# Performance work log

Measured on AMD Instinct MI355X. Metric: run time of the kernel, lower is better.

The kernel has to match this reference:

```python
import jax, jax.numpy as jnp
import numpy as np

B, N, F_IN, F_OUT = 8, 2048, 256, 256
NEG_SLOPE = 0.2
EPS = 1e-7


def setup_inputs() -> dict:
    key = jax.random.key(0)
    k1, k2, k3, k4, k5 = jax.random.split(key, 5)
    x = jax.random.normal(k1, (B, N, F_IN), dtype=jnp.float32)
    # A is a 0/1 adjacency mask used as float in the module
    A = jax.random.bernoulli(k2, 0.5, (B, N, N)).astype(jnp.float32)
    # W: xavier_normal_ init, shape [in_features, out_features]
    W = jax.random.normal(k3, (F_IN, F_OUT), dtype=jnp.float32) * np.sqrt(2.0 / (F_IN + F_OUT))
    # attention_mechanism: Linear(2*F_OUT, 1) -> weight vector [2*F_OUT], scalar bias
    bound = 1.0 / np.sqrt(2 * F_OUT)
    a_w = jax.random.uniform(k4, (2 * F_OUT,), dtype=jnp.float32, minval=-bound, maxval=bound)
    a_b = jax.random.uniform(k5, (), dtype=jnp.float32, minval=-bound, maxval=bound)
    return {"A": A, "x": x, "W": W, "a_w": a_w, "a_b": a_b}


def reference(A, x, W, a_w, a_b):
    # Wh = x @ W : [B, N, F_OUT]
    Wh = jnp.einsum('bnf,fo->bno', x, W)
    # Linear([Wh_i ; Wh_j]) == Wh_i @ a_w[:F] + Wh_j @ a_w[F:] + b  (no O(N^2 F) concat)
    s_src = Wh @ a_w[:F_OUT]   # [B, N] contribution of row index i
    s_dst = Wh @ a_w[F_OUT:]   # [B, N] contribution of col index j
    e = s_src[:, :, None] + s_dst[:, None, :] + a_b  # [B, N, N]
    e = jnp.where(e > 0, e, NEG_SLOPE * e)           # leaky_relu(0.2)
    # masked softmax over dim=1 (as in the original module)
    exps = jnp.exp(e) * A
    sums = jnp.sum(exps, axis=1, keepdims=True) + EPS
    attn = exps / sums                                # [B, N, N]
    return jnp.einsum('bij,bjo->bio', attn, Wh)       # [B, N, F_OUT]
```

## Files before the change

### kernel.cpp

```cpp
#include <hip/hip_runtime.h>
#include <hip/hip_bf16.h>

#define NN 2048
#define BB 8
#define FD 256
#define NEG_SLOPE 0.2f
#define EPSV 1e-7f
#define PSTR 36

typedef __bf16 bf16x8 __attribute__((ext_vector_type(8)));
typedef __bf16 bf16x4 __attribute__((ext_vector_type(4)));
typedef float f32x4 __attribute__((ext_vector_type(4)));

__device__ __forceinline__ void gload16(const __bf16* g, __bf16* l) {
    __builtin_amdgcn_global_load_lds((const __attribute__((address_space(1))) unsigned int*)g,
                                     (__attribute__((address_space(3))) unsigned int*)l,
                                     16, 0, 0);
}

__global__ __launch_bounds__(256) void k1_prep(const float* __restrict__ W,
                                               __bf16* __restrict__ WT) {
    int idx = blockIdx.x * 256 + threadIdx.x;
    int o = idx >> 8, f = idx & 255;
    WT[idx] = (__bf16)W[f * FD + o];
}

__global__ __launch_bounds__(256) void k2_whgemm(const float* __restrict__ x,
                                                 const __bf16* __restrict__ WT,
                                                 const float* __restrict__ a_w,
                                                 float* __restrict__ Wh,
                                                 float* __restrict__ s_src,
                                                 float* __restrict__ s_dst) {
    const int wave = threadIdx.x >> 6;
    const int lane = threadIdx.x & 63;
    const int row0 = blockIdx.x * 32 + (wave >> 1) * 16;
    const int ohalf = (wave & 1) * 128;
    const int m = lane & 15;
    const int quad = lane >> 4;
    const int row = row0 + m;
    const float* xrow = x + (size_t)row * FD + quad * 8;

    f32x4 acc[8];
#pragma unroll
    for (int n = 0; n < 8; ++n) acc[n] = (f32x4){0.f, 0.f, 0.f, 0.f};

    for (int k0 = 0; k0 < FD; k0 += 32) {
        float4 xa = *(const float4*)(xrow + k0);
        float4 xb = *(const float4*)(xrow + k0 + 4);
        bf16x8 af;
        af[0] = (__bf16)xa.x; af[1] = (__bf16)xa.y; af[2] = (__bf16)xa.z; af[3] = (__bf16)xa.w;
        af[4] = (__bf16)xb.x; af[5] = (__bf16)xb.y; af[6] = (__bf16)xb.z; af[7] = (__bf16)xb.w;
#pragma unroll
        for (int n = 0; n < 8; ++n) {
            int o = ohalf + n * 16 + m;
            bf16x8 bf = *(const bf16x8*)(WT + o * FD + k0 + quad * 8);
            acc[n] = __builtin_amdgcn_mfma_f32_16x16x32_bf16(af, bf, acc[n], 0, 0, 0);
        }
    }
#pragma unroll
    for (int n = 0; n < 8; ++n) {
        int o = ohalf + n * 16 + m;
#pragma unroll
        for (int r = 0; r < 4; ++r) {
            Wh[(size_t)(row0 + quad * 4 + r) * FD + o] = acc[n][r];
        }
    }

    float psrc[4] = {0.f, 0.f, 0.f, 0.f};
    float pdst[4] = {0.f, 0.f, 0.f, 0.f};
#pragma unroll
    for (int n = 0; n < 8; ++n) {
        int o = ohalf + n * 16 + m;
        float awS = a_w[o], awD = a_w[FD + o];
#pragma unroll
        for (int r = 0; r < 4; ++r) {
            psrc[r] += acc[n][r] * awS;
            pdst[r] += acc[n][r] * awD;
        }
    }
#pragma unroll
    for (int off = 1; off <= 8; off <<= 1) {
#pragma unroll
        for (int r = 0; r < 4; ++r) {
            psrc[r] += __shfl_xor(psrc[r], off, 64);
            pdst[r] += __shfl_xor(pdst[r], off, 64);
        }
    }
    __shared__ float sS[2][2][16], sD[2][2][16];
    if (m == 0) {
        int rp = wave >> 1, oh = wave & 1;
#pragma unroll
        for (int r = 0; r < 4; ++r) {
            sS[rp][oh][quad * 4 + r] = psrc[r];
            sD[rp][oh][quad * 4 + r] = pdst[r];
        }
    }
    __syncthreads();
    if (threadIdx.x < 32) {
        int rp = threadIdx.x >> 4, idx = threadIdx.x & 15;
        int orow = blockIdx.x * 32 + rp * 16 + idx;
        s_src[orow] = sS[rp][0][idx] + sS[rp][1][idx];
        s_dst[orow] = sD[rp][0][idx] + sD[rp][1][idx];
    }
}

__global__ __launch_bounds__(256) void k4_den(const float* __restrict__ A,
                                              const float* __restrict__ s_src,
                                              const float* __restrict__ s_dst,
                                              const float* __restrict__ a_bp,
                                              float* __restrict__ den_part) {
    const int blk = blockIdx.x;
    const int b = blk & 7;
    const int jhalf = (blk >> 3) & 1;
    const int isp = blk >> 4;
    const int i0 = isp * 32;
    const int j = jhalf * 1024 + threadIdx.x * 4;
    __shared__ float ss[32];
    if (threadIdx.x < 32) ss[threadIdx.x] = s_src[b * NN + i0 + threadIdx.x] + a_bp[0];
    __syncthreads();
    float4 sd = *(const float4*)(s_dst + b * NN + j);
    float ax = 0.f, ay = 0.f, az = 0.f, aw = 0.f;
    const float* Ap = A + ((size_t)b * NN + i0) * NN + j;
#pragma unroll 8
    for (int i = 0; i < 32; ++i) {
        float4 a = *(const float4*)(Ap + (size_t)i * NN);
        float si = ss[i];
        float e0 = si + sd.x; e0 = e0 > 0.f ? e0 : NEG_SLOPE * e0;
        float e1 = si + sd.y; e1 = e1 > 0.f ? e1 : NEG_SLOPE * e1;
        float e2 = si + sd.z; e2 = e2 > 0.f ? e2 : NEG_SLOPE * e2;
        float e3 = si + sd.w; e3 = e3 > 0.f ? e3 : NEG_SLOPE * e3;
        ax += a.x * __expf(e0);
        ay += a.y * __expf(e1);
        az += a.z * __expf(e2);
        aw += a.w * __expf(e3);
    }
    float4 r = (float4){ax, ay, az, aw};
    *(float4*)(den_part + (size_t)isp * (BB * NN) + b * NN + j) = r;
}

__global__ __launch_bounds__(256) void k5_wht(const float* __restrict__ Wh,
                                              const float* __restrict__ den_part,
                                              __bf16* __restrict__ WhT) {
    const int b = blockIdx.z;
    const int j0 = blockIdx.x * 64;
    const int o0 = blockIdx.y * 64;
    __shared__ float tile[64][65];
    __shared__ float invd[64];
    if (threadIdx.x < 64) {
        float s = 0.f;
        const float* dp = den_part + b * NN + j0 + threadIdx.x;
#pragma unroll 8
        for (int sI = 0; sI < 64; ++sI) s += dp[(size_t)sI * (BB * NN)];
        invd[threadIdx.x] = 1.f / (s + EPSV);
    }
    __syncthreads();
    int jr = threadIdx.x >> 4, oc = (threadIdx.x & 15) * 4;
#pragma unroll
    for (int p = 0; p < 4; ++p) {
        int jj = jr + p * 16;
        float4 v = *(const float4*)(Wh + (size_t)(b * NN + j0 + jj) * FD + o0 + oc);
        float s = invd[jj];
        tile[jj][oc + 0] = v.x * s;
        tile[jj][oc + 1] = v.y * s;
        tile[jj][oc + 2] = v.z * s;
        tile[jj][oc + 3] = v.w * s;
    }
    __syncthreads();
    int ow = threadIdx.x >> 4, jc = (threadIdx.x & 15) * 4;
#pragma unroll
    for (int p = 0; p < 4; ++p) {
        int o = ow + p * 16;
        bf16x4 wv;
        wv[0] = (__bf16)tile[jc + 0][o];
        wv[1] = (__bf16)tile[jc + 1][o];
        wv[2] = (__bf16)tile[jc + 2][o];
        wv[3] = (__bf16)tile[jc + 3][o];
        *(bf16x4*)(WhT + (size_t)(b * FD + o0 + o) * NN + j0 + jc) = wv;
    }
}

__global__ __launch_bounds__(256) void k6_out(const float* __restrict__ A,
                                              const __bf16* __restrict__ WhT,
                                              const float* __restrict__ s_src,
                                              const float* __restrict__ s_dst,
                                              const float* __restrict__ a_bp,
                                              float* __restrict__ out) {
    __shared__ __bf16 Pt[2][32 * PSTR];
    __shared__ __bf16 Bt[2][128 * 32];
    const int blk = blockIdx.x;
    const int b = blk & 7;
    const int r_ = blk >> 3;
    const int itile = r_ & 63;
    const int oh = r_ >> 6;
    const int i0 = itile * 32;
    const int o0 = oh * 128;
    const int t = threadIdx.x;
    const int w = t >> 6, lane = t & 63;
    const int m = lane & 15, quad = lane >> 4;
    const int wrow = w >> 1, wcol = w & 1;

    const int prow = t >> 3, pj = (t & 7) * 4;
    const float ssr = s_src[b * NN + i0 + prow] + a_bp[0];
    const float* Abase = A + ((size_t)(b * NN + i0 + prow)) * NN + pj;
    const float* sdbase = s_dst + b * NN + pj;
    __bf16* Pw = &Pt[0][0] + prow * PSTR + pj;
    const int pstep = 32 * PSTR;

    const __bf16* gB0 = WhT + ((size_t)(b * FD + o0 + w * 16 + (lane >> 2))) * NN + (lane & 3) * 8;
    const __bf16* gB1 = gB0 + (size_t)64 * NN;
    __bf16* lB0 = &Bt[0][0] + (w * 16) * 32;
    __bf16* lB1 = &Bt[0][0] + (w * 16 + 64) * 32;
    const int lstepB = 128 * 32;

    float4 a0 = *(const float4*)(Abase);
    float4 q0 = *(const float4*)(sdbase);
    gload16(gB0, lB0);
    gload16(gB1, lB1);

#define BUILD_P(dstbuf)                                                          \
    {                                                                            \
        bf16x4 pv; float e;                                                      \
        e = ssr + q0.x; e = e > 0.f ? e : NEG_SLOPE * e; pv[0] = (__bf16)(a0.x * __expf(e)); \
        e = ssr + q0.y; e = e > 0.f ? e : NEG_SLOPE * e; pv[1] = (__bf16)(a0.y * __expf(e)); \
        e = ssr + q0.z; e = e > 0.f ? e : NEG_SLOPE * e; pv[2] = (__bf16)(a0.z * __expf(e)); \
        e = ssr + q0.w; e = e > 0.f ? e : NEG_SLOPE * e; pv[3] = (__bf16)(a0.w * __expf(e)); \
        *(bf16x4*)(Pw + (dstbuf) * pstep) = pv;                                  \
    }

    BUILD_P(0)

    f32x4 acc[4];
#pragma unroll
    for (int n = 0; n < 4; ++n) acc[n] = (f32x4){0.f, 0.f, 0.f, 0.f};

    const __bf16* Pr = &Pt[0][0] + (wrow * 16 + m) * PSTR + quad * 8;
    const __bf16* Br = &Bt[0][0] + (wcol * 64 + m) * 32 + quad * 8;

    for (int kk = 0; kk < 64; ++kk) {
        __syncthreads();
        const int cur = kk & 1, nb = cur ^ 1;
        if (kk < 63) {
            gload16(gB0 + (kk + 1) * 32, lB0 + nb * lstepB);
            gload16(gB1 + (kk + 1) * 32, lB1 + nb * lstepB);
            a0 = *(const float4*)(Abase + (kk + 1) * 32);
            q0 = *(const float4*)(sdbase + (kk + 1) * 32);
        }
        const __bf16* Pk = Pr + cur * pstep;
        const __bf16* Bk = Br + cur * lstepB;
        bf16x8 af = *(const bf16x8*)(Pk);
#pragma unroll
        for (int n = 0; n < 4; ++n) {
            bf16x8 bfr = *(const bf16x8*)(Bk + n * 16 * 32);
            acc[n] = __builtin_amdgcn_mfma_f32_16x16x32_bf16(af, bfr, acc[n], 0, 0, 0);
        }
        if (kk < 63) BUILD_P(nb)
    }

#pragma unroll
    for (int n = 0; n < 4; ++n) {
        int o = o0 + wcol * 64 + n * 16 + m;
#pragma unroll
        for (int rr = 0; rr < 4; ++rr) {
            int orow = i0 + wrow * 16 + quad * 4 + rr;
            out[((size_t)b * NN + orow) * FD + o] = acc[n][rr];
        }
    }
#undef BUILD_P
}

extern "C" void kernel_launch(void* const* d_in, const int* in_sizes, int n_in,
                              void* d_out, int out_size, void* d_ws, size_t ws_size,
                              hipStream_t stream) {
    const float* A   = (const float*)d_in[0];
    const float* x   = (const float*)d_in[1];
    const float* W   = (const float*)d_in[2];
    const float* a_w = (const float*)d_in[3];
    const float* a_b = (const float*)d_in[4];
    float* out = (float*)d_out;

    char* ws = (char*)d_ws;
    __bf16* WT      = (__bf16*)ws;
    float*  Wh      = (float*)(ws + 131072);
    __bf16* WhT     = (__bf16*)(ws + 16908288);
    float*  s_src   = (float*)(ws + 25296896);
    float*  s_dst   = (float*)(ws + 25362432);
    float*  den_part= (float*)(ws + 25427968);

    k1_prep<<<256, 256, 0, stream>>>(W, WT);
    k2_whgemm<<<512, 256, 0, stream>>>(x, WT, a_w, Wh, s_src, s_dst);
    k4_den<<<1024, 256, 0, stream>>>(A, s_src, s_dst, a_b, den_part);
    k5_wht<<<dim3(32, 4, 8), 256, 0, stream>>>(Wh, den_part, WhT);
    k6_out<<<1024, 256, 0, stream>>>(A, WhT, s_src, s_dst, a_b, out);
}
```

Baseline: 297.8 us.

## Materialize bf16 attention matrix per batch pair and run separate tiled GEMM

```diff
diff --git a/kernel.cpp b/kernel.cpp
--- a/kernel.cpp
+++ b/kernel.cpp
@@ -6,7 +6,6 @@
 #define FD 256
 #define NEG_SLOPE 0.2f
 #define EPSV 1e-7f
-#define PSTR 36
 
 typedef __bf16 bf16x8 __attribute__((ext_vector_type(8)));
 typedef __bf16 bf16x4 __attribute__((ext_vector_type(4)));
@@ -104,15 +103,18 @@
     }
 }
 
-__global__ __launch_bounds__(256) void k4_den(const float* __restrict__ A,
-                                              const float* __restrict__ s_src,
-                                              const float* __restrict__ s_dst,
-                                              const float* __restrict__ a_bp,
-                                              float* __restrict__ den_part) {
+template <bool WD, bool WP>
+__global__ __launch_bounds__(256) void k4_t(const float* __restrict__ A,
+                                            const float* __restrict__ s_src,
+                                            const float* __restrict__ s_dst,
+                                            const float* __restrict__ a_bp,
+                                            float* __restrict__ den_part,
+                                            __bf16* __restrict__ P,
+                                            int bmask, int sh) {
     const int blk = blockIdx.x;
-    const int b = blk & 7;
-    const int jhalf = (blk >> 3) & 1;
-    const int isp = blk >> 4;
+    const int b = blk & bmask;
+    const int jhalf = (blk >> sh) & 1;
+    const int isp = blk >> (sh + 1);
     const int i0 = isp * 32;
     const int j = jhalf * 1024 + threadIdx.x * 4;
     __shared__ float ss[32];
@@ -121,7 +123,8 @@
     float4 sd = *(const float4*)(s_dst + b * NN + j);
     float ax = 0.f, ay = 0.f, az = 0.f, aw = 0.f;
     const float* Ap = A + ((size_t)b * NN + i0) * NN + j;
-#pragma unroll 8
+    __bf16* Pp = WP ? (P + ((size_t)b * NN + i0) * NN + j) : (__bf16*)0;
+#pragma unroll 4
     for (int i = 0; i < 32; ++i) {
         float4 a = *(const float4*)(Ap + (size_t)i * NN);
         float si = ss[i];
@@ -129,13 +132,22 @@
         float e1 = si + sd.y; e1 = e1 > 0.f ? e1 : NEG_SLOPE * e1;
         float e2 = si + sd.z; e2 = e2 > 0.f ? e2 : NEG_SLOPE * e2;
         float e3 = si + sd.w; e3 = e3 > 0.f ? e3 : NEG_SLOPE * e3;
-        ax += a.x * __expf(e0);
-        ay += a.y * __expf(e1);
-        az += a.z * __expf(e2);
-        aw += a.w * __expf(e3);
-    }
-    float4 r = (float4){ax, ay, az, aw};
-    *(float4*)(den_part + (size_t)isp * (BB * NN) + b * NN + j) = r;
+        float p0 = a.x * __expf(e0);
+        float p1 = a.y * __expf(e1);
+        float p2 = a.z * __expf(e2);
+        float p3 = a.w * __expf(e3);
+        if (WD) { ax += p0; ay += p1; az += p2; aw += p3; }
+        if (WP) {
+            bf16x4 pv;
+            pv[0] = (__bf16)p0; pv[1] = (__bf16)p1;
+            pv[2] = (__bf16)p2; pv[3] = (__bf16)p3;
+            *(bf16x4*)(Pp + (size_t)i * NN) = pv;
+        }
+    }
+    if (WD) {
+        float4 r = (float4){ax, ay, az, aw};
+        *(float4*)(den_part + (size_t)isp * (BB * NN) + b * NN + j) = r;
+    }
 }
 
 __global__ __launch_bounds__(256) void k5_wht(const float* __restrict__ Wh,
@@ -179,93 +191,81 @@
     }
 }
 
-__global__ __launch_bounds__(256) void k6_out(const float* __restrict__ A,
-                                              const __bf16* __restrict__ WhT,
-                                              const float* __restrict__ s_src,
-                                              const float* __restrict__ s_dst,
-                                              const float* __restrict__ a_bp,
-                                              float* __restrict__ out) {
-    __shared__ __bf16 Pt[2][32 * PSTR];
-    __shared__ __bf16 Bt[2][128 * 32];
+__global__ __launch_bounds__(256) void k6_gemm(const __bf16* __restrict__ P,
+                                               const __bf16* __restrict__ WhT,
+                                               float* __restrict__ out,
+                                               int bmask, int bsh) {
+    __shared__ __bf16 lA[2][64 * 64];
+    __shared__ __bf16 lB[2][128 * 64];
     const int blk = blockIdx.x;
-    const int b = blk & 7;
-    const int r_ = blk >> 3;
-    const int itile = r_ & 63;
-    const int oh = r_ >> 6;
-    const int i0 = itile * 32;
-    const int o0 = oh * 128;
+    const int b = blk & bmask;
+    const int r_ = blk >> bsh;
+    const int mt = r_ & 31;
+    const int nh = r_ >> 5;
+    const int i0 = mt * 64;
+    const int o0 = nh * 128;
     const int t = threadIdx.x;
     const int w = t >> 6, lane = t & 63;
     const int m = lane & 15, quad = lane >> 4;
-    const int wrow = w >> 1, wcol = w & 1;
-
-    const int prow = t >> 3, pj = (t & 7) * 4;
-    const float ssr = s_src[b * NN + i0 + prow] + a_bp[0];
-    const float* Abase = A + ((size_t)(b * NN + i0 + prow)) * NN + pj;
-    const float* sdbase = s_dst + b * NN + pj;
-    __bf16* Pw = &Pt[0][0] + prow * PSTR + pj;
-    const int pstep = 32 * PSTR;
-
-    const __bf16* gB0 = WhT + ((size_t)(b * FD + o0 + w * 16 + (lane >> 2))) * NN + (lane & 3) * 8;
-    const __bf16* gB1 = gB0 + (size_t)64 * NN;
-    __bf16* lB0 = &Bt[0][0] + (w * 16) * 32;
-    __bf16* lB1 = &Bt[0][0] + (w * 16 + 64) * 32;
-    const int lstepB = 128 * 32;
-
-    float4 a0 = *(const float4*)(Abase);
-    float4 q0 = *(const float4*)(sdbase);
-    gload16(gB0, lB0);
-    gload16(gB1, lB1);
-
-#define BUILD_P(dstbuf)                                                          \
-    {                                                                            \
-        bf16x4 pv; float e;                                                      \
-        e = ssr + q0.x; e = e > 0.f ? e : NEG_SLOPE * e; pv[0] = (__bf16)(a0.x * __expf(e)); \
-        e = ssr + q0.y; e = e > 0.f ? e : NEG_SLOPE * e; pv[1] = (__bf16)(a0.y * __expf(e)); \
-        e = ssr + q0.z; e = e > 0.f ? e : NEG_SLOPE * e; pv[2] = (__bf16)(a0.z * __expf(e)); \
-        e = ssr + q0.w; e = e > 0.f ? e : NEG_SLOPE * e; pv[3] = (__bf16)(a0.w * __expf(e)); \
-        *(bf16x4*)(Pw + (dstbuf) * pstep) = pv;                                  \
-    }
-
-    BUILD_P(0)
-
-    f32x4 acc[4];
-#pragma unroll
-    for (int n = 0; n < 4; ++n) acc[n] = (f32x4){0.f, 0.f, 0.f, 0.f};
-
-    const __bf16* Pr = &Pt[0][0] + (wrow * 16 + m) * PSTR + quad * 8;
-    const __bf16* Br = &Bt[0][0] + (wcol * 64 + m) * 32 + quad * 8;
-
-    for (int kk = 0; kk < 64; ++kk) {
+    const int wr = w >> 1, wc = w & 1;
+
+    const int srow = lane >> 3;
+    const int schunk = (lane & 7) ^ srow;
+    const __bf16* gA = P + ((size_t)(b * NN + i0 + w * 8 + srow)) * NN + schunk * 8;
+    const __bf16* gB = WhT + ((size_t)(b * FD + o0 + w * 8 + srow)) * NN + schunk * 8;
+
+#define STAGE6(buf, step) { \
+        const __bf16* ga = gA + (step) * 64; \
+        const __bf16* gb = gB + (step) * 64; \
+        gload16(ga,                   &lA[buf][0] + (w * 8) * 64); \
+        gload16(ga + (size_t)32 * NN, &lA[buf][0] + (32 + w * 8) * 64); \
+        gload16(gb,                   &lB[buf][0] + (w * 8) * 64); \
+        gload16(gb + (size_t)32 * NN, &lB[buf][0] + (32 + w * 8) * 64); \
+        gload16(gb + (size_t)64 * NN, &lB[buf][0] + (64 + w * 8) * 64); \
+        gload16(gb + (size_t)96 * NN, &lB[buf][0] + (96 + w * 8) * 64); \
+    }
+
+    STAGE6(0, 0)
+
+    f32x4 acc[2][4];
+#pragma unroll
+    for (int mi = 0; mi < 2; ++mi)
+#pragma unroll
+        for (int n = 0; n < 4; ++n) acc[mi][n] = (f32x4){0.f, 0.f, 0.f, 0.f};
+
+    const int swz = (m & 7) * 8;
+    for (int kt = 0; kt < 32; ++kt) {
         __syncthreads();
-        const int cur = kk & 1, nb = cur ^ 1;
-        if (kk < 63) {
-            gload16(gB0 + (kk + 1) * 32, lB0 + nb * lstepB);
-            gload16(gB1 + (kk + 1) * 32, lB1 + nb * lstepB);
-            a0 = *(const float4*)(Abase + (kk + 1) * 32);
-            q0 = *(const float4*)(sdbase + (kk + 1) * 32);
-        }
-        const __bf16* Pk = Pr + cur * pstep;
-        const __bf16* Bk = Br + cur * lstepB;
-        bf16x8 af = *(const bf16x8*)(Pk);
+        const int cur = kt & 1, nb = cur ^ 1;
+        if (kt < 31) STAGE6(nb, kt + 1)
+        const __bf16* lAc = &lA[cur][0];
+        const __bf16* lBc = &lB[cur][0];
+#pragma unroll
+        for (int ks = 0; ks < 2; ++ks) {
+            const int kof = (ks * 32 + quad * 8) ^ swz;
+            bf16x8 a0 = *(const bf16x8*)(lAc + (wr * 32 + m) * 64 + kof);
+            bf16x8 a1 = *(const bf16x8*)(lAc + (wr * 32 + 16 + m) * 64 + kof);
+#pragma unroll
+            for (int n = 0; n < 4; ++n) {
+                bf16x8 bfr = *(const bf16x8*)(lBc + (wc * 64 + n * 16 + m) * 64 + kof);
+                acc[0][n] = __builtin_amdgcn_mfma_f32_16x16x32_bf16(a0, bfr, acc[0][n], 0, 0, 0);
+                acc[1][n] = __builtin_amdgcn_mfma_f32_16x16x32_bf16(a1, bfr, acc[1][n], 0, 0, 0);
+            }
+        }
+    }
+
+#pragma unroll
+    for (int mi = 0; mi < 2; ++mi)
 #pragma unroll
         for (int n = 0; n < 4; ++n) {
-            bf16x8 bfr = *(const bf16x8*)(Bk + n * 16 * 32);
-            acc[n] = __builtin_amdgcn_mfma_f32_16x16x32_bf16(af, bfr, acc[n], 0, 0, 0);
-        }
-        if (kk < 63) BUILD_P(nb)
-    }
-
-#pragma unroll
-    for (int n = 0; n < 4; ++n) {
-        int o = o0 + wcol * 64 + n * 16 + m;
-#pragma unroll
-        for (int rr = 0; rr < 4; ++rr) {
-            int orow = i0 + wrow * 16 + quad * 4 + rr;
-            out[((size_t)b * NN + orow) * FD + o] = acc[n][rr];
-        }
-    }
-#undef BUILD_P
+            int o = o0 + wc * 64 + n * 16 + m;
+#pragma unroll
+            for (int rr = 0; rr < 4; ++rr) {
+                int orow = i0 + wr * 32 + mi * 16 + quad * 4 + rr;
+                out[((size_t)b * NN + orow) * FD + o] = acc[mi][n][rr];
+            }
+        }
+#undef STAGE6
 }
 
 extern "C" void kernel_launch(void* const* d_in, const int* in_sizes, int n_in,
@@ -288,7 +288,20 @@
 
     k1_prep<<<256, 256, 0, stream>>>(W, WT);
     k2_whgemm<<<512, 256, 0, stream>>>(x, WT, a_w, Wh, s_src, s_dst);
-    k4_den<<<1024, 256, 0, stream>>>(A, s_src, s_dst, a_b, den_part);
+
+    k4_t<true, false><<<1024, 256, 0, stream>>>(A, s_src, s_dst, a_b,
+                                                den_part, WhT, 7, 3);
     k5_wht<<<dim3(32, 4, 8), 256, 0, stream>>>(Wh, den_part, WhT);
-    k6_out<<<1024, 256, 0, stream>>>(A, WhT, s_src, s_dst, a_b, out);
-}
+
+    __bf16* Ppair = (__bf16*)Wh;
+    for (int c = 0; c < 4; ++c) {
+        const float* Ac  = A + (size_t)2 * c * NN * NN;
+        const float* ssc = s_src + (size_t)2 * c * NN;
+        const float* sdc = s_dst + (size_t)2 * c * NN;
+        k4_t<false, true><<<256, 256, 0, stream>>>(Ac, ssc, sdc, a_b,
+                                                   den_part, Ppair, 1, 1);
+        k6_gemm<<<128, 256, 0, stream>>>(Ppair,
+                                         WhT + (size_t)2 * c * FD * NN,
+                                         out + (size_t)2 * c * NN * FD, 1, 1);
+    }
+}
```

After: 380.1 us. 27.6% more time.
